# Kernel optimization log

Measured on AMD Instinct MI355X. Metric: run time of the kernel, lower is better.

Reference implementation:

```python
import jax, jax.numpy as jnp
import numpy as np

B = 1024   # env batch (rollout step, T=1)
F = 512    # feature_size ('big' conv tower)
H = 128    # LSTM hidden size


def _conv(x, W, b, stride):
    # x: [B,Cin,H,W], W: [Cout,Cin,kh,kw]  (PyTorch NCHW / OIHW, VALID padding)
    y = jax.lax.conv_general_dilated(x, W, (stride, stride), 'VALID',
                                     dimension_numbers=('NCHW', 'OIHW', 'NCHW'))
    return y + b[None, :, None, None]


def _tower(x, W1, b1, W2, b2, W3, b3, Wl, bl):
    y = jax.nn.relu(_conv(x, W1, b1, 4))   # [B,32,20,20]
    y = jax.nn.relu(_conv(y, W2, b2, 2))   # [B,64,9,9]
    y = jax.nn.relu(_conv(y, W3, b3, 1))   # [B,64,7,7]
    y = y.reshape(y.shape[0], -1)          # [B,3136]
    return jax.nn.relu(y @ Wl.T + bl)      # [B,512]


def _ln(x, g, b):
    m = jnp.mean(x, -1, keepdims=True)
    v = jnp.var(x, -1, keepdims=True)
    return (x - m) * jax.lax.rsqrt(v + 1e-5) * g + b


def setup_inputs() -> dict:
    key = jax.random.key(0)
    ks = iter(jax.random.split(key, 64))
    rn = lambda shape, s=0.05: jax.random.normal(next(ks), shape, jnp.float32) * s
    inp = {
        'x': jax.random.normal(next(ks), (B, 2, 84, 84), jnp.float32),
        'done': (jax.random.uniform(next(ks), (B,)) < 0.1).astype(jnp.float32),
        'h0': rn((1, B, H), 0.1),
        'c0': rn((1, B, H), 0.1),
        # video tower
        'vW1': rn((32, 1, 8, 8)), 'vb1': jnp.zeros((32,), jnp.float32),
        'vW2': rn((64, 32, 4, 4)), 'vb2': jnp.zeros((64,), jnp.float32),
        'vW3': rn((64, 64, 3, 3)), 'vb3': jnp.zeros((64,), jnp.float32),
        'vWl': rn((F, 64 * 7 * 7)), 'vbl': jnp.zeros((F,), jnp.float32),
        # audio tower
        'aW1': rn((32, 1, 8, 8)), 'ab1': jnp.zeros((32,), jnp.float32),
        'aW2': rn((64, 32, 4, 4)), 'ab2': jnp.zeros((64,), jnp.float32),
        'aW3': rn((64, 64, 3, 3)), 'ab3': jnp.zeros((64,), jnp.float32),
        'aWl': rn((F, 64 * 7 * 7)), 'abl': jnp.zeros((F,), jnp.float32),
        # LayerNorms
        'vln_g': jnp.ones((F,), jnp.float32), 'vln_b': jnp.zeros((F,), jnp.float32),
        'aln_g': jnp.ones((F,), jnp.float32), 'aln_b': jnp.zeros((F,), jnp.float32),
        # CASL attention
        'att_vW': rn((32, F)), 'att_vb': jnp.zeros((32,), jnp.float32),
        'att_aW': rn((32, F)), 'att_ab': jnp.zeros((32,), jnp.float32),
        'att_sW': rn((32, H)), 'att_sb': jnp.zeros((32,), jnp.float32),
        'attW': rn((2, 32)), 'attb': jnp.zeros((2,), jnp.float32),
        # LSTM (PyTorch gate order i,f,g,o)
        'Wih': rn((4 * H, F)), 'Whh': rn((4 * H, H)),
        'bih': jnp.zeros((4 * H,), jnp.float32), 'bhh': jnp.zeros((4 * H,), jnp.float32),
    }
    return inp


def reference(x, done, h0, c0,
              vW1, vb1, vW2, vb2, vW3, vb3, vWl, vbl,
              aW1, ab1, aW2, ab2, aW3, ab3, aWl, abl,
              vln_g, vln_b, aln_g, aln_b,
              att_vW, att_vb, att_aW, att_ab, att_sW, att_sb, attW, attb,
              Wih, Whh, bih, bhh):
    # get_states with T=1 rollout step (batch_size = B)
    vf = _ln(_tower(x[:, 0:1], vW1, vb1, vW2, vb2, vW3, vb3, vWl, vbl), vln_g, vln_b)  # [B,512]
    af = _ln(_tower(x[:, 1:2], aW1, ab1, aW2, ab2, aW3, ab3, aWl, abl), aln_g, aln_b)  # [B,512]
    # attention gating
    act = jnp.tanh(vf @ att_vW.T + att_vb + af @ att_aW.T + att_ab
                   + h0[0] @ att_sW.T + att_sb)                    # [B,32]
    w = jax.nn.softmax(act @ attW.T + attb, axis=-1)               # [B,2]
    fused = w[:, 0:1] * vf + w[:, 1:2] * af                        # [B,512]
    # done-masked LSTM cell (single timestep)
    m = (1.0 - done)[:, None]
    h = m * h0[0]
    c = m * c0[0]
    gates = fused @ Wih.T + bih + h @ Whh.T + bhh                  # [B,512]
    i, f, g, o = jnp.split(gates, 4, axis=-1)
    c_new = jax.nn.sigmoid(f) * c + jax.nn.sigmoid(i) * jnp.tanh(g)
    h_new = jax.nn.sigmoid(o) * jnp.tanh(c_new)                    # [B,128]
    return h_new, c_new, vf, af
```

## Files before the change

### kernel.cpp

```cpp
#include <hip/hip_runtime.h>


typedef unsigned short u16;
typedef unsigned int u32;
typedef __attribute__((ext_vector_type(8))) short bf16x8;
typedef __attribute__((ext_vector_type(4))) short bf16x4;
typedef __attribute__((ext_vector_type(4))) float f32x4;

__device__ __forceinline__ float b2f(u16 u) {
    union { u32 i; float f; } v; v.i = ((u32)u) << 16; return v.f;
}
__device__ __forceinline__ u16 f2b(float f) {
    union { float f; u32 i; } v; v.f = f;
    u32 r = v.i + 0x7fffu + ((v.i >> 16) & 1u);
    return (u16)(r >> 16);
}

__device__ __forceinline__ void gl_lds16(const u16* g, u16* l) {
    __builtin_amdgcn_global_load_lds(
        (const __attribute__((address_space(1))) void*)g,
        (__attribute__((address_space(3))) void*)l,
        16, 0, 0);
}

__device__ __forceinline__ int swz(int byte) {
    return byte ^ (((byte >> 7) & 7) << 4);
}

__global__ __launch_bounds__(256, 4) void tower_fused(
    const float* __restrict__ x,
    const u16* __restrict__ Wp1, const u16* __restrict__ Wp2,
    const u16* __restrict__ Wp3,
    const float* __restrict__ vb1, const float* __restrict__ ab1,
    const float* __restrict__ vb2, const float* __restrict__ ab2,
    const float* __restrict__ vb3, const float* __restrict__ ab3,
    u16* __restrict__ c3f)
{
    __shared__ __attribute__((aligned(16))) u16 scratch[84 * 84];
    __shared__ __attribute__((aligned(16))) u16 c1L[400 * 32];

    const int tid = threadIdx.x;
    const int wave = tid >> 6, lane = tid & 63, quad = lane >> 4, l16 = lane & 15;
    const int bl = blockIdx.x, t = blockIdx.y;

    const u16* Wpt1 = Wp1 + t * 2048;
    const u16* Wpt2 = Wp2 + t * 32768;
    const u16* Wpt3 = Wp3 + t * 36864;

    bf16x8 bw[2][2];
#pragma unroll
    for (int ks = 0; ks < 2; ++ks)
#pragma unroll
        for (int ni = 0; ni < 2; ++ni)
            bw[ks][ni] = *(const bf16x8*)(Wpt1 + ((ks * 2 + ni) * 64 + lane) * 8);

    {
        const float* xim = x + ((long)bl * 2 + t) * 7056;
#pragma unroll
        for (int it = 0; it < 7; ++it) {
            const int e4 = (tid + it * 256) * 4;
            if (e4 < 7056) {
                float4 v = *(const float4*)(xim + e4);
                bf16x4 s;
                s[0] = (short)f2b(v.x); s[1] = (short)f2b(v.y);
                s[2] = (short)f2b(v.z); s[3] = (short)f2b(v.w);
                *(bf16x4*)(scratch + e4) = s;
            }
        }
    }
    __syncthreads();

    {
        const float* b1 = t ? ab1 : vb1;
        const float bv0 = b1[l16], bv1 = b1[16 + l16];

        for (int tile = wave; tile < 25; tile += 4) {
            const int m = tile * 16 + l16;
            const int oy = m / 20, ox = m % 20;
            const u16* base = scratch + (oy * 4) * 84 + ox * 4;
            const u16* ap0 = base + (quad) * 84;
            const u16* ap1 = base + (4 + quad) * 84;
            bf16x4 lo0 = *(const bf16x4*)(ap0);
            bf16x4 hi0 = *(const bf16x4*)(ap0 + 4);
            bf16x4 lo1 = *(const bf16x4*)(ap1);
            bf16x4 hi1 = *(const bf16x4*)(ap1 + 4);
            bf16x8 a0, a1;
#pragma unroll
            for (int j = 0; j < 4; ++j) {
                a0[j] = lo0[j]; a0[4 + j] = hi0[j];
                a1[j] = lo1[j]; a1[4 + j] = hi1[j];
            }
            f32x4 acc0 = (f32x4){0.f, 0.f, 0.f, 0.f};
            f32x4 acc1 = (f32x4){0.f, 0.f, 0.f, 0.f};
            acc0 = __builtin_amdgcn_mfma_f32_16x16x32_bf16(a0, bw[0][0], acc0, 0, 0, 0);
            acc1 = __builtin_amdgcn_mfma_f32_16x16x32_bf16(a0, bw[0][1], acc1, 0, 0, 0);
            acc0 = __builtin_amdgcn_mfma_f32_16x16x32_bf16(a1, bw[1][0], acc0, 0, 0, 0);
            acc1 = __builtin_amdgcn_mfma_f32_16x16x32_bf16(a1, bw[1][1], acc1, 0, 0, 0);
#pragma unroll
            for (int rr = 0; rr < 4; ++rr) {
                const int row = tile * 16 + quad * 4 + rr;
                *(u16*)((char*)c1L + swz((row * 32 + l16) * 2)) =
                    f2b(fmaxf(acc0[rr] + bv0, 0.f));
                *(u16*)((char*)c1L + swz((row * 32 + 16 + l16) * 2)) =
                    f2b(fmaxf(acc1[rr] + bv1, 0.f));
            }
        }
    }

    bf16x8 wb[2][4];
#pragma unroll
    for (int ni = 0; ni < 4; ++ni)
        wb[0][ni] = *(const bf16x8*)(Wpt2 + ((0 * 4 + ni) * 64 + lane) * 8);

    __syncthreads();

    {
        const float* b2 = t ? ab2 : vb2;
        float bv[4];
#pragma unroll
        for (int ni = 0; ni < 4; ++ni) bv[ni] = b2[ni * 16 + l16];

        const int t0 = wave;
        const int t1 = wave + 4;
        const bool has2 = (t1 < 6);

        const int m0 = t0 * 16 + l16;
        const int oyA = m0 / 9, oxA = m0 % 9;
        const int baseA = ((oyA * 2) * 20 + oxA * 2) * 64 + quad * 16;
        int m1 = t1 * 16 + l16; if (m1 > 80) m1 = 80;
        const int oyB = m1 / 9, oxB = m1 % 9;
        const int baseB = ((oyB * 2) * 20 + oxB * 2) * 64 + quad * 16;

        f32x4 accA[4], accB[4];
#pragma unroll
        for (int ni = 0; ni < 4; ++ni) {
            accA[ni] = (f32x4){0.f, 0.f, 0.f, 0.f};
            accB[ni] = (f32x4){0.f, 0.f, 0.f, 0.f};
        }

        bf16x8 aA[2], aB[2];
        {
            aA[0] = *(const bf16x8*)((const char*)c1L + swz(baseA));
            if (has2) aB[0] = *(const bf16x8*)((const char*)c1L + swz(baseB));
        }

#pragma unroll
        for (int pp = 0; pp < 16; ++pp) {
            const int cur = pp & 1, nxt = cur ^ 1;
            if (pp + 1 < 16) {
                const int pn = pp + 1;
                const int kyn = pn >> 2, kxn = pn & 3;
                const int poffn = (kyn * 20 + kxn) * 64;
#pragma unroll
                for (int ni = 0; ni < 4; ++ni)
                    wb[nxt][ni] = *(const bf16x8*)(Wpt2 + ((pn * 4 + ni) * 64 + lane) * 8);
                aA[nxt] = *(const bf16x8*)((const char*)c1L + swz(baseA + poffn));
                if (has2)
                    aB[nxt] = *(const bf16x8*)((const char*)c1L + swz(baseB + poffn));
            }
#pragma unroll
            for (int ni = 0; ni < 4; ++ni)
                accA[ni] = __builtin_amdgcn_mfma_f32_16x16x32_bf16(aA[cur], wb[cur][ni], accA[ni], 0, 0, 0);
            if (has2) {
#pragma unroll
                for (int ni = 0; ni < 4; ++ni)
                    accB[ni] = __builtin_amdgcn_mfma_f32_16x16x32_bf16(aB[cur], wb[cur][ni], accB[ni], 0, 0, 0);
            }
        }

        u16* c2L = scratch;
#pragma unroll
        for (int ni = 0; ni < 4; ++ni)
#pragma unroll
            for (int rr = 0; rr < 4; ++rr) {
                const int r0 = t0 * 16 + quad * 4 + rr;
                c2L[r0 * 72 + ni * 16 + l16] = f2b(fmaxf(accA[ni][rr] + bv[ni], 0.f));
            }
        if (has2) {
#pragma unroll
            for (int ni = 0; ni < 4; ++ni)
#pragma unroll
                for (int rr = 0; rr < 4; ++rr) {
                    const int r1 = t1 * 16 + quad * 4 + rr;
                    if (r1 < 81)
                        c2L[r1 * 72 + ni * 16 + l16] = f2b(fmaxf(accB[ni][rr] + bv[ni], 0.f));
                }
        }
    }

    bf16x8 w3[2][4];
#pragma unroll
    for (int ni = 0; ni < 4; ++ni)
        w3[0][ni] = *(const bf16x8*)(Wpt3 + ((0 * 4 + ni) * 64 + lane) * 8);

    __syncthreads();

    {
        const float* b3 = t ? ab3 : vb3;
        float bv[4];
#pragma unroll
        for (int ni = 0; ni < 4; ++ni) bv[ni] = b3[ni * 16 + l16];

        int m = wave * 16 + l16; if (m > 48) m = 48;
        const int oy = m / 7, ox = m % 7;
        const u16* c2L = scratch;
        const u16* base = c2L + (oy * 9 + ox) * 72 + quad * 8;

        f32x4 acc[4];
#pragma unroll
        for (int ni = 0; ni < 4; ++ni) acc[ni] = (f32x4){0.f, 0.f, 0.f, 0.f};

        bf16x8 aa[2];
        aa[0] = *(const bf16x8*)(base);

#pragma unroll
        for (int cc = 0; cc < 18; ++cc) {
            const int cur = cc & 1, nxt = cur ^ 1;
            if (cc + 1 < 18) {
                const int cn = cc + 1;
                const int cpix = cn >> 1, ksn = cn & 1;
                const int kyn = cpix / 3, kxn = cpix % 3;
#pragma unroll
                for (int ni = 0; ni < 4; ++ni)
                    w3[nxt][ni] = *(const bf16x8*)(Wpt3 + ((cn * 4 + ni) * 64 + lane) * 8);
                aa[nxt] = *(const bf16x8*)(base + (kyn * 9 + kxn) * 72 + ksn * 32);
            }
#pragma unroll
            for (int ni = 0; ni < 4; ++ni)
                acc[ni] = __builtin_amdgcn_mfma_f32_16x16x32_bf16(aa[cur], w3[cur][ni], acc[ni], 0, 0, 0);
        }

        u16* outp = c3f + ((long)t * 1024 + bl) * 3136;
#pragma unroll
        for (int ni = 0; ni < 4; ++ni)
#pragma unroll
            for (int rr = 0; rr < 4; ++rr) {
                const int row = wave * 16 + quad * 4 + rr;
                if (row < 49)
                    outp[row * 64 + ni * 16 + l16] = f2b(fmaxf(acc[ni][rr] + bv[ni], 0.f));
            }
    }
}

__global__ __launch_bounds__(256) void gemm_skp(
    const u16* __restrict__ A, const u16* __restrict__ B0,
    const u16* __restrict__ B1,
    float* __restrict__ Cp, int M, int Mhalf, int N, int K, int Kc)
{
    __shared__ __attribute__((aligned(16))) u16 As[128 * 32];
    __shared__ __attribute__((aligned(16))) u16 Bs[128 * 32];

    const int tid  = threadIdx.x;
    const int wave = tid >> 6, lane = tid & 63;
    const int quad = lane >> 4, l16 = lane & 15;
    const int m0 = blockIdx.y * 128, n0 = blockIdx.x * 128;
    const u16* B = (m0 < Mhalf) ? B0 : B1;
    const int wm = (wave >> 1) * 64, wn = (wave & 1) * 64;
    const int kfrom = blockIdx.z * Kc;
    int kto = kfrom + Kc; if (kto > K) kto = K;
    float* C = Cp + (long)blockIdx.z * M * N;

    const int rl = lane >> 2, sg = lane & 3;
    const u16* gA0 = A + (long)(m0 + wave * 32 + rl) * K + kfrom + sg * 8;
    const u16* gA1 = A + (long)(m0 + wave * 32 + 16 + rl) * K + kfrom + sg * 8;
    const u16* gB0 = B + (long)(n0 + wave * 32 + rl) * K + kfrom + sg * 8;
    const u16* gB1 = B + (long)(n0 + wave * 32 + 16 + rl) * K + kfrom + sg * 8;
    u16* lA = As + wave * 1024;
    u16* lB = Bs + wave * 1024;

    f32x4 acc[4][4];
#pragma unroll
    for (int mi = 0; mi < 4; ++mi)
#pragma unroll
        for (int ni = 0; ni < 4; ++ni)
            acc[mi][ni] = (f32x4){0.f, 0.f, 0.f, 0.f};

    for (int koff = 0; koff < kto - kfrom; koff += 32) {
        gl_lds16(gA0 + koff, lA);
        gl_lds16(gA1 + koff, lA + 512);
        gl_lds16(gB0 + koff, lB);
        gl_lds16(gB1 + koff, lB + 512);
        __syncthreads();

        bf16x8 af[4], bfr[4];
#pragma unroll
        for (int mi = 0; mi < 4; ++mi)
            af[mi] = *(const bf16x8*)(As + (wm + mi * 16 + l16) * 32 + quad * 8);
#pragma unroll
        for (int ni = 0; ni < 4; ++ni)
            bfr[ni] = *(const bf16x8*)(Bs + (wn + ni * 16 + l16) * 32 + quad * 8);
#pragma unroll
        for (int mi = 0; mi < 4; ++mi)
#pragma unroll
            for (int ni = 0; ni < 4; ++ni)
                acc[mi][ni] = __builtin_amdgcn_mfma_f32_16x16x32_bf16(
                    af[mi], bfr[ni], acc[mi][ni], 0, 0, 0);
        __syncthreads();
    }

#pragma unroll
    for (int mi = 0; mi < 4; ++mi)
#pragma unroll
        for (int ni = 0; ni < 4; ++ni) {
            int col = n0 + wn + ni * 16 + l16;
#pragma unroll
            for (int rr = 0; rr < 4; ++rr) {
                int row = m0 + wm + mi * 16 + quad * 4 + rr;
                C[(long)row * N + col] = acc[mi][ni][rr];
            }
        }
}

__global__ __launch_bounds__(256) void pack_all(
    const float* __restrict__ vWl, const float* __restrict__ aWl,
    const float* __restrict__ vW1, const float* __restrict__ aW1,
    const float* __restrict__ vW2, const float* __restrict__ aW2,
    const float* __restrict__ vW3, const float* __restrict__ aW3,
    const float* __restrict__ avW, const float* __restrict__ aaW,
    const float* __restrict__ asW,
    const float* __restrict__ Wih, const float* __restrict__ Whh,
    u16* __restrict__ Wlb,
    u16* __restrict__ Wp1, u16* __restrict__ Wp2, u16* __restrict__ Wp3,
    u16* __restrict__ WTatt, u16* __restrict__ Bcat)
{
    __shared__ float row[3136];
    const int bid = blockIdx.x, tid = threadIdx.x;

    if (bid < 1024) {
        const int n = bid & 511;
        const float* src = (bid < 512) ? vWl : aWl;
        for (int i = tid; i < 3136; i += 256)
            row[i] = src[(long)n * 3136 + i];
        __syncthreads();
        u16* d = Wlb + (long)bid * 3136;
        for (int i = tid; i < 3136; i += 256) {
            int p = i >> 6, oc = i & 63;
            d[i] = f2b(row[oc * 49 + p]);
        }
        return;
    }

    const int idx = (bid - 1024) * 256 + tid;
    if (idx < 4096) {
        const float* s = (idx < 2048) ? vW1 : aW1;
        int j0 = idx & 2047;
        int jj = j0 & 7, lane = (j0 >> 3) & 63, rest = j0 >> 9;
        int ni = rest & 1, ks = rest >> 1;
        int oc = ni * 16 + (lane & 15);
        int k  = ks * 32 + (lane >> 4) * 8 + jj;
        Wp1[idx] = f2b(s[oc * 64 + k]);
    } else if (idx < 69632) {
        int i = idx - 4096;
        const float* s = (i < 32768) ? vW2 : aW2;
        int j0 = i & 32767;
        int jj = j0 & 7, lane = (j0 >> 3) & 63, rest = j0 >> 9;
        int ni = rest & 3, rest2 = rest >> 2;
        int ks = rest2 & 1, c = rest2 >> 1;
        int oc = ni * 16 + (lane & 15);
        int k  = c * 64 + ks * 32 + (lane >> 4) * 8 + jj;
        int pos = k >> 5, ic = k & 31;
        int ky = pos >> 2, kx = pos & 3;
        Wp2[i] = f2b(s[((oc * 32 + ic) * 4 + ky) * 4 + kx]);
    } else if (idx < 143360) {
        int i = idx - 69632;
        const float* s = (i < 36864) ? vW3 : aW3;
        int j0 = i % 36864;
        int jj = j0 & 7, lane = (j0 >> 3) & 63, rest = j0 >> 9;
        int ni = rest & 3, rest2 = rest >> 2;
        int ks = rest2 & 1, c = rest2 >> 1;
        int oc = ni * 16 + (lane & 15);
        int k  = c * 64 + ks * 32 + (lane >> 4) * 8 + jj;
        int pos = k >> 6, ic = k & 63;
        int ky = pos / 3, kx = pos % 3;
        Wp3[i] = f2b(s[((oc * 64 + ic) * 3 + ky) * 3 + kx]);
    } else if (idx < 180224) {
        int i = idx - 143360;
        int k = i >> 5, j = i & 31;
        float v = (k < 512) ? avW[(long)j * 512 + k]
                : (k < 1024) ? aaW[(long)j * 512 + (k - 512)]
                : asW[(long)j * 128 + (k - 1024)];
        WTatt[i] = f2b(v);
    } else if (idx < 507904) {
        int i = idx - 180224;
        int n = i / 640, k = i % 640;
        Bcat[i] = f2b((k < 512) ? Wih[(long)n * 512 + k]
                                : Whh[(long)n * 128 + (k - 512)]);
    }
}

__global__ __launch_bounds__(256) void ln_attn(
    const float* __restrict__ ychp,
    const float* __restrict__ bl_v, const float* __restrict__ bl_a,
    const float* __restrict__ g_v,  const float* __restrict__ g_a,
    const float* __restrict__ be_v, const float* __restrict__ be_a,
    const float* __restrict__ h0,   const float* __restrict__ done,
    const u16* __restrict__ WT,
    const float* __restrict__ avb, const float* __restrict__ aab,
    const float* __restrict__ asb,
    const float* __restrict__ attW, const float* __restrict__ attb,
    float* __restrict__ vf_out, float* __restrict__ af_out,
    u16* __restrict__ Acat)
{
    __shared__ float vs[512], afs[512], hs[128], part[8][32], act[32], wsm[2];
    __shared__ float redS[4], redQ[4];
    const int b = blockIdx.x, tid = threadIdx.x;
    const int lane = tid & 63, wv = tid >> 6;

    if (tid < 128) hs[tid] = h0[b * 128 + tid];

#pragma unroll
    for (int tw = 0; tw < 2; ++tw) {
        const long row = tw ? (1024 + b) : b;
        const float* bias = tw ? bl_a : bl_v;
        const float* g    = tw ? g_a  : g_v;
        const float* be   = tw ? be_a : be_v;
        float* fo   = tw ? af_out : vf_out;
        float* dst  = tw ? afs : vs;

        float s0 = bias[tid], s1 = bias[tid + 256];
#pragma unroll
        for (int z = 0; z < 7; ++z) {
            const float* yr = ychp + (long)z * 1048576 + row * 512;
            s0 += yr[tid];
            s1 += yr[tid + 256];
        }
        float v0 = fmaxf(s0, 0.f), v1 = fmaxf(s1, 0.f);

        float sum = v0 + v1, sq = v0 * v0 + v1 * v1;
#pragma unroll
        for (int o = 32; o; o >>= 1) {
            sum += __shfl_xor(sum, o);
            sq  += __shfl_xor(sq, o);
        }
        if (lane == 0) { redS[wv] = sum; redQ[wv] = sq; }
        __syncthreads();
        const float ts = redS[0] + redS[1] + redS[2] + redS[3];
        const float tq = redQ[0] + redQ[1] + redQ[2] + redQ[3];
        const float mean = ts * (1.f / 512.f);
        const float var  = tq * (1.f / 512.f) - mean * mean;
        const float inv  = rsqrtf(var + 1e-5f);

        float o0 = (v0 - mean) * inv * g[tid]       + be[tid];
        float o1 = (v1 - mean) * inv * g[tid + 256] + be[tid + 256];
        dst[tid] = o0; dst[tid + 256] = o1;
        fo[(long)b * 512 + tid]       = o0;
        fo[(long)b * 512 + tid + 256] = o1;
        __syncthreads();
    }

    {
        const int j = tid & 31, g = tid >> 5;
        float a = 0.f;
#pragma unroll 8
        for (int k = g * 64; k < g * 64 + 64; ++k)
            a += vs[k] * b2f(WT[k * 32 + j]);
#pragma unroll 8
        for (int k = g * 64; k < g * 64 + 64; ++k)
            a += afs[k] * b2f(WT[(512 + k) * 32 + j]);
#pragma unroll 8
        for (int k = g * 16; k < g * 16 + 16; ++k)
            a += hs[k] * b2f(WT[(1024 + k) * 32 + j]);
        part[g][j] = a;
    }
    __syncthreads();
    if (tid < 32) {
        float a = avb[tid] + aab[tid] + asb[tid];
#pragma unroll
        for (int g2 = 0; g2 < 8; ++g2) a += part[g2][tid];
        act[tid] = tanhf(a);
    }
    __syncthreads();
    if (tid == 0) {
        float l0 = attb[0], l1 = attb[1];
        for (int j = 0; j < 32; ++j) {
            l0 += act[j] * attW[j];
            l1 += act[j] * attW[32 + j];
        }
        float mx = fmaxf(l0, l1);
        float e0 = expf(l0 - mx), e1 = expf(l1 - mx);
        float s = e0 + e1;
        wsm[0] = e0 / s; wsm[1] = e1 / s;
    }
    __syncthreads();
    const float w0 = wsm[0], w1 = wsm[1];
    const float m = 1.f - done[b];
    for (int i = tid; i < 512; i += 256)
        Acat[(long)b * 640 + i] = f2b(w0 * vs[i] + w1 * afs[i]);
    if (tid < 128)
        Acat[(long)b * 640 + 512 + tid] = f2b(m * hs[tid]);
}

__global__ __launch_bounds__(128) void lstm_fin(
    const float* __restrict__ gatesp,
    const float* __restrict__ bih, const float* __restrict__ bhh,
    const float* __restrict__ c0, const float* __restrict__ done,
    float* __restrict__ out)
{
    const int b = blockIdx.x, j = threadIdx.x;
    float gi = bih[j]       + bhh[j];
    float gf = bih[128 + j] + bhh[128 + j];
    float gg = bih[256 + j] + bhh[256 + j];
    float go = bih[384 + j] + bhh[384 + j];
#pragma unroll
    for (int z = 0; z < 4; ++z) {
        const float* G = gatesp + (long)z * 524288 + (long)b * 512;
        gi += G[j]; gf += G[128 + j]; gg += G[256 + j]; go += G[384 + j];
    }
    float m  = 1.f - done[b];
    float c  = m * c0[b * 128 + j];
    float si = 1.f / (1.f + expf(-gi));
    float sf = 1.f / (1.f + expf(-gf));
    float so = 1.f / (1.f + expf(-go));
    float cn = sf * c + si * tanhf(gg);
    float hn = so * tanhf(cn);
    out[b * 128 + j]          = hn;
    out[131072 + b * 128 + j] = cn;
}

extern "C" void kernel_launch(void* const* d_in, const int* in_sizes, int n_in,
                              void* d_out, int out_size, void* d_ws, size_t ws_size,
                              hipStream_t stream)
{
    (void)in_sizes; (void)n_in; (void)out_size; (void)ws_size;

    const float* x     = (const float*)d_in[0];
    const float* done  = (const float*)d_in[1];
    const float* h0    = (const float*)d_in[2];
    const float* c0in  = (const float*)d_in[3];
    const float* vW1   = (const float*)d_in[4];
    const float* vb1   = (const float*)d_in[5];
    const float* vW2   = (const float*)d_in[6];
    const float* vb2   = (const float*)d_in[7];
    const float* vW3   = (const float*)d_in[8];
    const float* vb3   = (const float*)d_in[9];
    const float* vWl   = (const float*)d_in[10];
    const float* vbl   = (const float*)d_in[11];
    const float* aW1   = (const float*)d_in[12];
    const float* ab1   = (const float*)d_in[13];
    const float* aW2   = (const float*)d_in[14];
    const float* ab2   = (const float*)d_in[15];
    const float* aW3   = (const float*)d_in[16];
    const float* ab3   = (const float*)d_in[17];
    const float* aWl   = (const float*)d_in[18];
    const float* abl   = (const float*)d_in[19];
    const float* vln_g = (const float*)d_in[20];
    const float* vln_b = (const float*)d_in[21];
    const float* aln_g = (const float*)d_in[22];
    const float* aln_b = (const float*)d_in[23];
    const float* att_vW = (const float*)d_in[24];
    const float* att_vb = (const float*)d_in[25];
    const float* att_aW = (const float*)d_in[26];
    const float* att_ab = (const float*)d_in[27];
    const float* att_sW = (const float*)d_in[28];
    const float* att_sb = (const float*)d_in[29];
    const float* attW  = (const float*)d_in[30];
    const float* attb  = (const float*)d_in[31];
    const float* Wih   = (const float*)d_in[32];
    const float* Whh   = (const float*)d_in[33];
    const float* bih   = (const float*)d_in[34];
    const float* bhh   = (const float*)d_in[35];

    float* out = (float*)d_out;
    float* vf_out = out + 262144;
    float* af_out = out + 786432;

    char* p = (char*)d_ws;
    float* gatesp = (float*)p; p += 4ul * 1024 * 512 * 4;
    float* ychp   = (float*)p; p += 7ul * 2048 * 512 * 4;
    u16*   Acat   = (u16*)p;   p += 1024ul * 640 * 2;
    u16*   Bcat   = (u16*)p;   p += 512ul * 640 * 2;
    u16*   Wlb    = (u16*)p;   p += 2ul * 512 * 3136 * 2;
    u16*   Wp1    = (u16*)p;   p += 2ul * 2048 * 2;
    u16*   Wp2    = (u16*)p;   p += 2ul * 32768 * 2;
    u16*   Wp3    = (u16*)p;   p += 2ul * 36864 * 2;
    u16*   WTatt  = (u16*)p;   p += 36864ul * 2;
    u16*   c3f    = (u16*)p;

    hipLaunchKernelGGL(pack_all, dim3(3008), dim3(256), 0, stream,
        vWl, aWl, vW1, aW1, vW2, aW2, vW3, aW3, att_vW, att_aW, att_sW,
        Wih, Whh, Wlb, Wp1, Wp2, Wp3, WTatt, Bcat);

    hipLaunchKernelGGL(tower_fused, dim3(1024, 2), dim3(256), 0, stream,
        x, Wp1, Wp2, Wp3, vb1, ab1, vb2, ab2, vb3, ab3, c3f);

    hipLaunchKernelGGL(gemm_skp, dim3(4, 16, 7), dim3(256), 0, stream,
        c3f, Wlb, Wlb + 512ul * 3136, ychp, 2048, 1024, 512, 3136, 448);

    hipLaunchKernelGGL(ln_attn, dim3(1024), dim3(256), 0, stream,
        ychp, vbl, abl, vln_g, aln_g, vln_b, aln_b, h0, done, WTatt,
        att_vb, att_ab, att_sb, attW, attb, vf_out, af_out, Acat);

    hipLaunchKernelGGL(gemm_skp, dim3(4, 8, 4), dim3(256), 0, stream,
        Acat, Bcat, Bcat, gatesp, 1024, 1 << 30, 512, 640, 160);

    hipLaunchKernelGGL(lstm_fin, dim3(1024), dim3(128), 0, stream,
        gatesp, bih, bhh, c0in, done, out);
}
```

Baseline: 250.9 us.

## Process two images per block in conv tower, two waves per image

The fused conv tower now handles two batch images per workgroup, with each pair of waves owning one image. The grid is halved and LDS buffers are doubled. Each wave now carries 3 conv2 tiles and 2 conv3 tiles instead of an uneven 1-2 and 1. This balances per-wave work (the old conv3 left wave 3 mostly idle) and reuses the weight fragments loaded from global across more MFMAs. In exchange it raises register and LDS use, so launch bounds drop to 2 blocks per CU, which may lower occupancy.

```diff
diff --git a/kernel.cpp b/kernel.cpp
--- a/kernel.cpp
+++ b/kernel.cpp
@@ -27,7 +27,7 @@
     return byte ^ (((byte >> 7) & 7) << 4);
 }
 
-__global__ __launch_bounds__(256, 4) void tower_fused(
+__global__ __launch_bounds__(256, 2) void tower_fused(
     const float* __restrict__ x,
     const u16* __restrict__ Wp1, const u16* __restrict__ Wp2,
     const u16* __restrict__ Wp3,
@@ -36,12 +36,13 @@
     const float* __restrict__ vb3, const float* __restrict__ ab3,
     u16* __restrict__ c3f)
 {
-    __shared__ __attribute__((aligned(16))) u16 scratch[84 * 84];
-    __shared__ __attribute__((aligned(16))) u16 c1L[400 * 32];
+    __shared__ __attribute__((aligned(16))) u16 scratch2[2 * 7056];
+    __shared__ __attribute__((aligned(16))) u16 c1L[2 * 400 * 32];
 
     const int tid = threadIdx.x;
     const int wave = tid >> 6, lane = tid & 63, quad = lane >> 4, l16 = lane & 15;
-    const int bl = blockIdx.x, t = blockIdx.y;
+    const int bl0 = blockIdx.x * 2, t = blockIdx.y;
+    const int wi = wave >> 1, lw = wave & 1;
 
     const u16* Wpt1 = Wp1 + t * 2048;
     const u16* Wpt2 = Wp2 + t * 32768;
@@ -54,8 +55,10 @@
         for (int ni = 0; ni < 2; ++ni)
             bw[ks][ni] = *(const bf16x8*)(Wpt1 + ((ks * 2 + ni) * 64 + lane) * 8);
 
-    {
-        const float* xim = x + ((long)bl * 2 + t) * 7056;
+#pragma unroll
+    for (int si = 0; si < 2; ++si) {
+        const float* xim = x + ((long)(bl0 + si) * 2 + t) * 7056;
+        u16* simg = scratch2 + si * 7056;
 #pragma unroll
         for (int it = 0; it < 7; ++it) {
             const int e4 = (tid + it * 256) * 4;
@@ -64,20 +67,23 @@
                 bf16x4 s;
                 s[0] = (short)f2b(v.x); s[1] = (short)f2b(v.y);
                 s[2] = (short)f2b(v.z); s[3] = (short)f2b(v.w);
-                *(bf16x4*)(scratch + e4) = s;
+                *(bf16x4*)(simg + e4) = s;
             }
         }
     }
     __syncthreads();
+
+    const u16* simg = scratch2 + wi * 7056;
+    const int imgb = wi * 25600;
 
     {
         const float* b1 = t ? ab1 : vb1;
         const float bv0 = b1[l16], bv1 = b1[16 + l16];
 
-        for (int tile = wave; tile < 25; tile += 4) {
+        for (int tile = lw; tile < 25; tile += 2) {
             const int m = tile * 16 + l16;
             const int oy = m / 20, ox = m % 20;
-            const u16* base = scratch + (oy * 4) * 84 + ox * 4;
+            const u16* base = simg + (oy * 4) * 84 + ox * 4;
             const u16* ap0 = base + (quad) * 84;
             const u16* ap1 = base + (4 + quad) * 84;
             bf16x4 lo0 = *(const bf16x4*)(ap0);
@@ -99,9 +105,9 @@
 #pragma unroll
             for (int rr = 0; rr < 4; ++rr) {
                 const int row = tile * 16 + quad * 4 + rr;
-                *(u16*)((char*)c1L + swz((row * 32 + l16) * 2)) =
+                *(u16*)((char*)c1L + imgb + swz((row * 32 + l16) * 2)) =
                     f2b(fmaxf(acc0[rr] + bv0, 0.f));
-                *(u16*)((char*)c1L + swz((row * 32 + 16 + l16) * 2)) =
+                *(u16*)((char*)c1L + imgb + swz((row * 32 + 16 + l16) * 2)) =
                     f2b(fmaxf(acc1[rr] + bv1, 0.f));
             }
         }
@@ -120,72 +126,59 @@
 #pragma unroll
         for (int ni = 0; ni < 4; ++ni) bv[ni] = b2[ni * 16 + l16];
 
-        const int t0 = wave;
-        const int t1 = wave + 4;
-        const bool has2 = (t1 < 6);
-
-        const int m0 = t0 * 16 + l16;
-        const int oyA = m0 / 9, oxA = m0 % 9;
-        const int baseA = ((oyA * 2) * 20 + oxA * 2) * 64 + quad * 16;
-        int m1 = t1 * 16 + l16; if (m1 > 80) m1 = 80;
-        const int oyB = m1 / 9, oxB = m1 % 9;
-        const int baseB = ((oyB * 2) * 20 + oxB * 2) * 64 + quad * 16;
-
-        f32x4 accA[4], accB[4];
-#pragma unroll
-        for (int ni = 0; ni < 4; ++ni) {
-            accA[ni] = (f32x4){0.f, 0.f, 0.f, 0.f};
-            accB[ni] = (f32x4){0.f, 0.f, 0.f, 0.f};
-        }
-
-        bf16x8 aA[2], aB[2];
-        {
-            aA[0] = *(const bf16x8*)((const char*)c1L + swz(baseA));
-            if (has2) aB[0] = *(const bf16x8*)((const char*)c1L + swz(baseB));
-        }
+        int bA[3];
+#pragma unroll
+        for (int j = 0; j < 3; ++j) {
+            int m = (lw * 3 + j) * 16 + l16; if (m > 80) m = 80;
+            const int oy = m / 9, ox = m % 9;
+            bA[j] = ((oy * 2) * 20 + ox * 2) * 64 + quad * 16;
+        }
+
+        f32x4 acc[3][4];
+#pragma unroll
+        for (int j = 0; j < 3; ++j)
+#pragma unroll
+            for (int ni = 0; ni < 4; ++ni)
+                acc[j][ni] = (f32x4){0.f, 0.f, 0.f, 0.f};
+
+        bf16x8 aA[3][2];
+#pragma unroll
+        for (int j = 0; j < 3; ++j)
+            aA[j][0] = *(const bf16x8*)((const char*)c1L + imgb + swz(bA[j]));
 
 #pragma unroll
         for (int pp = 0; pp < 16; ++pp) {
             const int cur = pp & 1, nxt = cur ^ 1;
             if (pp + 1 < 16) {
                 const int pn = pp + 1;
-                const int kyn = pn >> 2, kxn = pn & 3;
-                const int poffn = (kyn * 20 + kxn) * 64;
+                const int poffn = ((pn >> 2) * 20 + (pn & 3)) * 64;
 #pragma unroll
                 for (int ni = 0; ni < 4; ++ni)
                     wb[nxt][ni] = *(const bf16x8*)(Wpt2 + ((pn * 4 + ni) * 64 + lane) * 8);
-                aA[nxt] = *(const bf16x8*)((const char*)c1L + swz(baseA + poffn));
-                if (has2)
-                    aB[nxt] = *(const bf16x8*)((const char*)c1L + swz(baseB + poffn));
+#pragma unroll
+                for (int j = 0; j < 3; ++j)
+                    aA[j][nxt] = *(const bf16x8*)((const char*)c1L + imgb + swz(bA[j] + poffn));
             }
 #pragma unroll
+            for (int j = 0; j < 3; ++j)
+#pragma unroll
+                for (int ni = 0; ni < 4; ++ni)
+                    acc[j][ni] = __builtin_amdgcn_mfma_f32_16x16x32_bf16(
+                        aA[j][cur], wb[cur][ni], acc[j][ni], 0, 0, 0);
+        }
+
+        u16* c2L = scratch2 + wi * 5832;
+#pragma unroll
+        for (int j = 0; j < 3; ++j)
+#pragma unroll
             for (int ni = 0; ni < 4; ++ni)
-                accA[ni] = __builtin_amdgcn_mfma_f32_16x16x32_bf16(aA[cur], wb[cur][ni], accA[ni], 0, 0, 0);
-            if (has2) {
-#pragma unroll
-                for (int ni = 0; ni < 4; ++ni)
-                    accB[ni] = __builtin_amdgcn_mfma_f32_16x16x32_bf16(aB[cur], wb[cur][ni], accB[ni], 0, 0, 0);
-            }
-        }
-
-        u16* c2L = scratch;
-#pragma unroll
-        for (int ni = 0; ni < 4; ++ni)
-#pragma unroll
-            for (int rr = 0; rr < 4; ++rr) {
-                const int r0 = t0 * 16 + quad * 4 + rr;
-                c2L[r0 * 72 + ni * 16 + l16] = f2b(fmaxf(accA[ni][rr] + bv[ni], 0.f));
-            }
-        if (has2) {
-#pragma unroll
-            for (int ni = 0; ni < 4; ++ni)
 #pragma unroll
                 for (int rr = 0; rr < 4; ++rr) {
-                    const int r1 = t1 * 16 + quad * 4 + rr;
-                    if (r1 < 81)
-                        c2L[r1 * 72 + ni * 16 + l16] = f2b(fmaxf(accB[ni][rr] + bv[ni], 0.f));
+                    const int r = (lw * 3 + j) * 16 + quad * 4 + rr;
+                    if (r < 81)
+                        c2L[r * 72 + ni * 16 + l16] =
+                            f2b(fmaxf(acc[j][ni][rr] + bv[ni], 0.f));
                 }
-        }
     }
 
     bf16x8 w3[2][4];
@@ -201,17 +194,26 @@
 #pragma unroll
         for (int ni = 0; ni < 4; ++ni) bv[ni] = b3[ni * 16 + l16];
 
-        int m = wave * 16 + l16; if (m > 48) m = 48;
-        const int oy = m / 7, ox = m % 7;
-        const u16* c2L = scratch;
-        const u16* base = c2L + (oy * 9 + ox) * 72 + quad * 8;
-
-        f32x4 acc[4];
-#pragma unroll
-        for (int ni = 0; ni < 4; ++ni) acc[ni] = (f32x4){0.f, 0.f, 0.f, 0.f};
-
-        bf16x8 aa[2];
-        aa[0] = *(const bf16x8*)(base);
+        const u16* c2L = scratch2 + wi * 5832;
+        const u16* base3[2];
+#pragma unroll
+        for (int j = 0; j < 2; ++j) {
+            int m = (lw * 2 + j) * 16 + l16; if (m > 48) m = 48;
+            const int oy = m / 7, ox = m % 7;
+            base3[j] = c2L + (oy * 9 + ox) * 72 + quad * 8;
+        }
+
+        f32x4 acc3[2][4];
+#pragma unroll
+        for (int j = 0; j < 2; ++j)
+#pragma unroll
+            for (int ni = 0; ni < 4; ++ni)
+                acc3[j][ni] = (f32x4){0.f, 0.f, 0.f, 0.f};
+
+        bf16x8 aa[2][2];
+#pragma unroll
+        for (int j = 0; j < 2; ++j)
+            aa[j][0] = *(const bf16x8*)(base3[j]);
 
 #pragma unroll
         for (int cc = 0; cc < 18; ++cc) {
@@ -219,26 +221,34 @@
             if (cc + 1 < 18) {
                 const int cn = cc + 1;
                 const int cpix = cn >> 1, ksn = cn & 1;
-                const int kyn = cpix / 3, kxn = cpix % 3;
+                const int aoff = ((cpix / 3) * 9 + (cpix % 3)) * 72 + ksn * 32;
 #pragma unroll
                 for (int ni = 0; ni < 4; ++ni)
                     w3[nxt][ni] = *(const bf16x8*)(Wpt3 + ((cn * 4 + ni) * 64 + lane) * 8);
-                aa[nxt] = *(const bf16x8*)(base + (kyn * 9 + kxn) * 72 + ksn * 32);
+#pragma unroll
+                for (int j = 0; j < 2; ++j)
+                    aa[j][nxt] = *(const bf16x8*)(base3[j] + aoff);
             }
 #pragma unroll
+            for (int j = 0; j < 2; ++j)
+#pragma unroll
+                for (int ni = 0; ni < 4; ++ni)
+                    acc3[j][ni] = __builtin_amdgcn_mfma_f32_16x16x32_bf16(
+                        aa[j][cur], w3[cur][ni], acc3[j][ni], 0, 0, 0);
+        }
+
+        u16* outp = c3f + ((long)t * 1024 + bl0 + wi) * 3136;
+#pragma unroll
+        for (int j = 0; j < 2; ++j)
+#pragma unroll
             for (int ni = 0; ni < 4; ++ni)
-                acc[ni] = __builtin_amdgcn_mfma_f32_16x16x32_bf16(aa[cur], w3[cur][ni], acc[ni], 0, 0, 0);
-        }
-
-        u16* outp = c3f + ((long)t * 1024 + bl) * 3136;
-#pragma unroll
-        for (int ni = 0; ni < 4; ++ni)
-#pragma unroll
-            for (int rr = 0; rr < 4; ++rr) {
-                const int row = wave * 16 + quad * 4 + rr;
-                if (row < 49)
-                    outp[row * 64 + ni * 16 + l16] = f2b(fmaxf(acc[ni][rr] + bv[ni], 0.f));
-            }
+#pragma unroll
+                for (int rr = 0; rr < 4; ++rr) {
+                    const int row = (lw * 2 + j) * 16 + quad * 4 + rr;
+                    if (row < 49)
+                        outp[row * 64 + ni * 16 + l16] =
+                            f2b(fmaxf(acc3[j][ni][rr] + bv[ni], 0.f));
+                }
     }
 }
 
@@ -580,7 +590,7 @@
         vWl, aWl, vW1, aW1, vW2, aW2, vW3, aW3, att_vW, att_aW, att_sW,
         Wih, Whh, Wlb, Wp1, Wp2, Wp3, WTatt, Bcat);
 
-    hipLaunchKernelGGL(tower_fused, dim3(1024, 2), dim3(256), 0, stream,
+    hipLaunchKernelGGL(tower_fused, dim3(512, 2), dim3(256), 0, stream,
         x, Wp1, Wp2, Wp3, vb1, ab1, vb2, ab2, vb3, ab3, c3f);
 
     hipLaunchKernelGGL(gemm_skp, dim3(4, 16, 7), dim3(256), 0, stream,
```

Result: no change. 252.8 us (+0.8%).
